# Kernel optimization log

Measured on AMD Instinct MI355X. Metric: run time of the kernel, lower is better.

Reference implementation:

```python
import jax, jax.numpy as jnp
import numpy as np


def setup_inputs() -> dict:
    key = jax.random.key(0)
    k1, k2, k3 = jax.random.split(key, 3)
    B, T, D, H = 64, 512, 1024, 1024
    x = jax.random.normal(k1, (B, T, D), dtype=jnp.float32)
    state = jnp.zeros((B, H), dtype=jnp.float32)
    W = jax.random.normal(k2, (H, H), dtype=jnp.float32) / np.sqrt(H).astype(np.float32)
    U = jax.random.normal(k3, (D, H), dtype=jnp.float32) / np.sqrt(D).astype(np.float32)
    b = jnp.zeros((H,), dtype=jnp.float32)
    return {"x": x, "state": state, "W": W, "U": U, "b": b}


def reference(x, state, W, U, b):
    # x: (B, T, D) -> precompute input projection for all steps: (T, B, H)
    xU = jnp.einsum('btd,dh->tbh', x, U) + b

    def step(h, xu_t):
        h = jnp.tanh(xu_t + h @ W)
        return h, h

    final_state, outs = jax.lax.scan(step, state, xU)  # outs: (T, B, H)
    outs = jnp.transpose(outs, (1, 0, 2))  # (B, T, H)
    return outs, final_state
```

## Files before the change

### kernel.cpp

```cpp
#include <hip/hip_runtime.h>
#include <hip/hip_fp16.h>

typedef float  f4v __attribute__((ext_vector_type(4)));
typedef _Float16 h8v __attribute__((ext_vector_type(8)));
typedef _Float16 h4v __attribute__((ext_vector_type(4)));

#define B_ 64
#define T_ 512
#define H_ 1024

__global__ __launch_bounds__(256) void k_transpose_cvt(const float* __restrict__ src,
                                                       _Float16* __restrict__ dst) {
  __shared__ _Float16 tile[64][72];
  int r0 = blockIdx.y * 64, c0 = blockIdx.x * 64;
  int t = threadIdx.x;
  for (int i = 0; i < 4; ++i) {
    int r = i * 16 + (t >> 4);
    int c = (t & 15) * 4;
    f4v v = *reinterpret_cast<const f4v*>(src + (long)(r0 + r) * 1024 + c0 + c);
    tile[c + 0][r] = (_Float16)v.x;
    tile[c + 1][r] = (_Float16)v.y;
    tile[c + 2][r] = (_Float16)v.z;
    tile[c + 3][r] = (_Float16)v.w;
  }
  __syncthreads();
  for (int i = 0; i < 2; ++i) {
    int rr = i * 32 + (t >> 3);
    int cc = (t & 7) * 8;
    *reinterpret_cast<h8v*>(dst + (long)(c0 + rr) * 1024 + r0 + cc) =
        *reinterpret_cast<const h8v*>(&tile[rr][cc]);
  }
}

#define SWZG(r, kh) ((((r) * 64) + ((kh) * 2)) ^ (((r) & 3) << 4))

__global__ __launch_bounds__(256) void k_gemm_xu(const float* __restrict__ x,
                                                 const _Float16* __restrict__ Ut,
                                                 const float* __restrict__ bias,
                                                 float* __restrict__ out) {
  __shared__ __attribute__((aligned(16))) unsigned char Asm[128 * 32 * 2];
  __shared__ __attribute__((aligned(16))) unsigned char Bsm[128 * 32 * 2];
  int bid = blockIdx.x;
  int nt = bid & 7, mt = bid >> 3;
  int t = threadIdx.x;
  int row = t >> 1, kc = (t & 1) * 16;
  long gA = (long)(mt * 128 + row) * 1024 + kc;
  long gB = (long)(nt * 128 + row) * 1024 + kc;
  int wid = t >> 6, lane = t & 63;
  int wr = (wid >> 1) * 64, wc = (wid & 1) * 64;
  int l15 = lane & 15, khi = (lane >> 4) * 8;

  f4v acc[4][4];
  for (int i = 0; i < 4; ++i)
    for (int j = 0; j < 4; ++j) acc[i][j] = (f4v){0.f, 0.f, 0.f, 0.f};

  f4v ra[4];
  h8v rb[2];
  {
    const float* ap = x + gA;
    ra[0] = *(const f4v*)(ap);     ra[1] = *(const f4v*)(ap + 4);
    ra[2] = *(const f4v*)(ap + 8); ra[3] = *(const f4v*)(ap + 12);
    const _Float16* bp = Ut + gB;
    rb[0] = *(const h8v*)(bp);     rb[1] = *(const h8v*)(bp + 8);
  }
  for (int kt = 0; kt < 32; ++kt) {
    h8v ah0, ah1;
    for (int j = 0; j < 4; ++j) {
      ah0[j]     = (_Float16)ra[0][j];
      ah0[j + 4] = (_Float16)ra[1][j];
      ah1[j]     = (_Float16)ra[2][j];
      ah1[j + 4] = (_Float16)ra[3][j];
    }
    *(h8v*)(Asm + SWZG(row, kc))     = ah0;
    *(h8v*)(Asm + SWZG(row, kc + 8)) = ah1;
    *(h8v*)(Bsm + SWZG(row, kc))     = rb[0];
    *(h8v*)(Bsm + SWZG(row, kc + 8)) = rb[1];
    __syncthreads();
    if (kt < 31) {
      const float* ap = x + gA + (kt + 1) * 32;
      ra[0] = *(const f4v*)(ap);     ra[1] = *(const f4v*)(ap + 4);
      ra[2] = *(const f4v*)(ap + 8); ra[3] = *(const f4v*)(ap + 12);
      const _Float16* bp = Ut + gB + (kt + 1) * 32;
      rb[0] = *(const h8v*)(bp);     rb[1] = *(const h8v*)(bp + 8);
    }
    h8v af[4], bf[4];
    for (int mi = 0; mi < 4; ++mi)
      af[mi] = *(const h8v*)(Asm + SWZG(wr + mi * 16 + l15, khi));
    for (int ni = 0; ni < 4; ++ni)
      bf[ni] = *(const h8v*)(Bsm + SWZG(wc + ni * 16 + l15, khi));
    for (int mi = 0; mi < 4; ++mi)
      for (int ni = 0; ni < 4; ++ni)
        acc[mi][ni] = __builtin_amdgcn_mfma_f32_16x16x32_f16(af[mi], bf[ni], acc[mi][ni], 0, 0, 0);
    __syncthreads();
  }
  int coff = nt * 128 + wc, roff = mt * 128 + wr;
  for (int ni = 0; ni < 4; ++ni) {
    int col = coff + ni * 16 + l15;
    float bb = bias[col];
    for (int mi = 0; mi < 4; ++mi) {
      int rbase = roff + mi * 16 + (lane >> 4) * 4;
      for (int j = 0; j < 4; ++j)
        out[(long)(rbase + j) * 1024 + col] = acc[mi][ni][j] + bb;
    }
  }
}

#define SWZS(r, kh) ((((r) * 2048) + ((kh) * 2)) ^ (((r) & 7) << 4))

__global__ __launch_bounds__(256) void k_scan(const float* __restrict__ state,
                                              float* __restrict__ out,
                                              const _Float16* __restrict__ Wt,
                                              unsigned* __restrict__ ctr) {
  extern __shared__ __attribute__((aligned(16))) unsigned char smem[];
  unsigned char* Wl = smem;
  unsigned char* Hl0 = smem + 65536;
  __shared__ int fastflag;
  int t = threadIdx.x;
  int bid = blockIdx.x;
  int cl = bid & 7;
  int mm = bid >> 3;

  unsigned* stepc = ctr + cl * 32;
  unsigned* testc = ctr + 256 + cl * 32;
  unsigned* gbar  = ctr + 512;

  {
    int r = t >> 3, c8 = t & 7;
    const _Float16* wsrc = Wt + (long)(mm * 32 + r) * 1024;
    for (int j = 0; j < 16; ++j) {
      int kh = (c8 + 8 * j) * 8;
      *(h8v*)(Wl + SWZS(r, kh)) = *(const h8v*)(wsrc + kh);
    }
  }

  if (t == 0) {
    unsigned one = 1u, zero = 0u, got;
    asm volatile("global_atomic_add %0, %1, off\n\ts_waitcnt vmcnt(0)"
                 :: "v"(testc), "v"(one) : "memory");
    __hip_atomic_fetch_add(gbar, 1u, __ATOMIC_RELAXED, __HIP_MEMORY_SCOPE_AGENT);
    while (__hip_atomic_load(gbar, __ATOMIC_RELAXED, __HIP_MEMORY_SCOPE_AGENT) < 256u)
      __builtin_amdgcn_s_sleep(2);
    asm volatile("global_atomic_add %0, %1, %2, off sc0\n\ts_waitcnt vmcnt(0)"
                 : "=&v"(got) : "v"(testc), "v"(zero) : "memory");
    fastflag = (got == 32u);
  }
  __syncthreads();
  const bool fastm = (fastflag != 0);

  int wid = t >> 6, lane = t & 63;
  int srow = t >> 5, slane = t & 31;
  long b = cl * 8 + srow;
  int l15 = lane & 15, khi8 = (lane >> 4) * 8;
  int arow = lane & 7;
  int bro = wid * 16 + l15;
  int hi = lane >> 4;
  int gcol = mm * 32 + wid * 16 + l15;
  bool prod = (wid < 2) && (hi < 2);

  for (int step = 0; step < T_; ++step) {
    unsigned char* Hb = Hl0 + (step & 1) * 16384;

    float xuv[4];
    long addr0 = 0;
    if (prod) {
      addr0 = ((long)(cl * 8 + hi * 4) * T_ + step) * 1024 + gcol;
#pragma unroll
      for (int j = 0; j < 4; ++j) xuv[j] = out[addr0 + (long)j * T_ * 1024];
    }

    if (step == 0) {
      const float* hp0 = state + b * 1024 + slane * 4;
#pragma unroll
      for (int j = 0; j < 8; ++j) {
        f4v v = *(const f4v*)(hp0 + 128 * j);
        h4v hv = {(_Float16)v.x, (_Float16)v.y, (_Float16)v.z, (_Float16)v.w};
        *(h4v*)(Hb + SWZS(srow, (slane + 32 * j) * 4)) = hv;
      }
    } else {
      if (t == 0) {
        unsigned tgt = 32u * (unsigned)step;
        if (fastm) {
          unsigned cur, zero = 0u;
          do {
            asm volatile("global_atomic_add %0, %1, %2, off sc0\n\ts_waitcnt vmcnt(0)"
                         : "=&v"(cur) : "v"(stepc), "v"(zero) : "memory");
          } while (cur < tgt);
        } else {
          while (__hip_atomic_load(stepc, __ATOMIC_RELAXED, __HIP_MEMORY_SCOPE_AGENT) < tgt)
            __builtin_amdgcn_s_sleep(1);
        }
      }
      __syncthreads();

      const float* hrow = out + (b * T_ + (step - 1)) * 1024;
      if (fastm) {
#pragma unroll
        for (int j = 0; j < 8; ++j) {
          int c0 = (slane + 32 * j) * 4;
          if ((c0 >> 5) == mm) continue;
          f4v v = *(const f4v*)(hrow + c0);
          h4v hv = {(_Float16)v.x, (_Float16)v.y, (_Float16)v.z, (_Float16)v.w};
          *(h4v*)(Hb + SWZS(srow, c0)) = hv;
        }
      } else {
        const float* hp = hrow + slane * 4;
        f4v w0, w1, w2, w3, w4, w5, w6, w7;
        asm volatile(
            "global_load_dwordx4 %0, %8, off sc0 sc1\n\t"
            "global_load_dwordx4 %1, %8, off offset:512 sc0 sc1\n\t"
            "global_load_dwordx4 %2, %8, off offset:1024 sc0 sc1\n\t"
            "global_load_dwordx4 %3, %8, off offset:1536 sc0 sc1\n\t"
            "global_load_dwordx4 %4, %8, off offset:2048 sc0 sc1\n\t"
            "global_load_dwordx4 %5, %8, off offset:2560 sc0 sc1\n\t"
            "global_load_dwordx4 %6, %8, off offset:3072 sc0 sc1\n\t"
            "global_load_dwordx4 %7, %8, off offset:3584 sc0 sc1\n\t"
            "s_waitcnt vmcnt(0)"
            : "=&v"(w0), "=&v"(w1), "=&v"(w2), "=&v"(w3),
              "=&v"(w4), "=&v"(w5), "=&v"(w6), "=&v"(w7)
            : "v"(hp)
            : "memory");
        f4v wv[8] = {w0, w1, w2, w3, w4, w5, w6, w7};
#pragma unroll
        for (int j = 0; j < 8; ++j) {
          int c0 = (slane + 32 * j) * 4;
          h4v hv = {(_Float16)wv[j][0], (_Float16)wv[j][1],
                    (_Float16)wv[j][2], (_Float16)wv[j][3]};
          *(h4v*)(Hb + SWZS(srow, c0)) = hv;
        }
      }
    }
    __syncthreads();

    if (wid < 2) {
      f4v ac0 = (f4v){0.f, 0.f, 0.f, 0.f}, ac1 = ac0, ac2 = ac0, ac3 = ac0;
#pragma unroll
      for (int s = 0; s < 32; s += 4) {
        int k0 = s * 32 + khi8, k1 = k0 + 32, k2 = k0 + 64, k3 = k0 + 96;
        h8v af0 = *(const h8v*)(Hb + SWZS(arow, k0));
        h8v bf0 = *(const h8v*)(Wl + SWZS(bro, k0));
        h8v af1 = *(const h8v*)(Hb + SWZS(arow, k1));
        h8v bf1 = *(const h8v*)(Wl + SWZS(bro, k1));
        h8v af2 = *(const h8v*)(Hb + SWZS(arow, k2));
        h8v bf2 = *(const h8v*)(Wl + SWZS(bro, k2));
        h8v af3 = *(const h8v*)(Hb + SWZS(arow, k3));
        h8v bf3 = *(const h8v*)(Wl + SWZS(bro, k3));
        ac0 = __builtin_amdgcn_mfma_f32_16x16x32_f16(af0, bf0, ac0, 0, 0, 0);
        ac1 = __builtin_amdgcn_mfma_f32_16x16x32_f16(af1, bf1, ac1, 0, 0, 0);
        ac2 = __builtin_amdgcn_mfma_f32_16x16x32_f16(af2, bf2, ac2, 0, 0, 0);
        ac3 = __builtin_amdgcn_mfma_f32_16x16x32_f16(af3, bf3, ac3, 0, 0, 0);
      }
      f4v acc = (ac0 + ac1) + (ac2 + ac3);
      if (hi < 2) {
        float v0 = tanhf(acc[0] + xuv[0]);
        float v1 = tanhf(acc[1] + xuv[1]);
        float v2 = tanhf(acc[2] + xuv[2]);
        float v3 = tanhf(acc[3] + xuv[3]);
        float* p0 = out + addr0;
        float* p1 = p0 + (long)T_ * 1024;
        float* p2 = p1 + (long)T_ * 1024;
        float* p3 = p2 + (long)T_ * 1024;
        if (fastm) {
          p0[0] = v0; p1[0] = v1; p2[0] = v2; p3[0] = v3;
        } else {
          asm volatile(
              "global_store_dword %0, %4, off sc0 sc1\n\t"
              "global_store_dword %1, %5, off sc0 sc1\n\t"
              "global_store_dword %2, %6, off sc0 sc1\n\t"
              "global_store_dword %3, %7, off sc0 sc1\n\t"
              "s_waitcnt vmcnt(0)"
              :: "v"(p0), "v"(p1), "v"(p2), "v"(p3),
                 "v"(v0), "v"(v1), "v"(v2), "v"(v3)
              : "memory");
        }
        if (step < T_ - 1) {
          unsigned char* Hn = Hl0 + ((step + 1) & 1) * 16384;
          int cb = gcol & ~3, co = (gcol & 3) * 2;
          int r0r = hi * 4;
          *(_Float16*)(Hn + SWZS(r0r + 0, cb) + co) = (_Float16)v0;
          *(_Float16*)(Hn + SWZS(r0r + 1, cb) + co) = (_Float16)v1;
          *(_Float16*)(Hn + SWZS(r0r + 2, cb) + co) = (_Float16)v2;
          *(_Float16*)(Hn + SWZS(r0r + 3, cb) + co) = (_Float16)v3;
        }
        if (step == T_ - 1) {
          long r = (long)cl * 8 + hi * 4;
          float* q = out + (long)B_ * T_ * 1024 + r * 1024 + gcol;
          q[0] = v0; q[1024] = v1; q[2048] = v2; q[3072] = v3;
        }
      }
    }

    if (prod) {
      asm volatile("s_waitcnt vmcnt(0)" ::: "memory");
    }
    __syncthreads();
    if (t == 0) {
      if (fastm) {
        unsigned one = 1u;
        asm volatile("global_atomic_add %0, %1, off" :: "v"(stepc), "v"(one) : "memory");
      } else {
        __hip_atomic_fetch_add(stepc, 1u, __ATOMIC_RELAXED, __HIP_MEMORY_SCOPE_AGENT);
      }
    }
  }
}

extern "C" void kernel_launch(void* const* d_in, const int* in_sizes, int n_in,
                              void* d_out, int out_size, void* d_ws, size_t ws_size,
                              hipStream_t stream) {
  const float* x     = (const float*)d_in[0];
  const float* state = (const float*)d_in[1];
  const float* W     = (const float*)d_in[2];
  const float* U     = (const float*)d_in[3];
  const float* bias  = (const float*)d_in[4];
  float* out = (float*)d_out;
  unsigned char* ws = (unsigned char*)d_ws;

  _Float16* Ut = (_Float16*)ws;
  _Float16* Wt = (_Float16*)(ws + (1u << 21));
  unsigned* ctr = (unsigned*)(ws + (1u << 22));

  hipMemsetAsync(ctr, 0, 4096, stream);

  k_transpose_cvt<<<dim3(16, 16), 256, 0, stream>>>(U, Ut);
  k_transpose_cvt<<<dim3(16, 16), 256, 0, stream>>>(W, Wt);
  k_gemm_xu<<<2048, 256, 0, stream>>>(x, Ut, bias, out);

  hipFuncSetAttribute((const void*)k_scan, hipFuncAttributeMaxDynamicSharedMemorySize, 98304);
  void* args[] = {(void*)&state, (void*)&out, (void*)&Wt, (void*)&ctr};
  hipLaunchCooperativeKernel((void*)k_scan, dim3(256), dim3(256), args, 98304, stream);
}
```

Before: 1.880 ms.

## Replace per-step counter polling with sharded counters and leader-broadcast flags

In the fast path, the per-cluster step barrier changes. Arrivals are spread across four counters instead of one. Only block mm==0 polls those counters, then writes a per-block flag that the other 31 blocks spin on. This cuts atomic contention from 32 pollers hammering one address, but it adds an extra hop of latency through the leader's flag writes. The final step also skips its arrival increment.

```diff
diff --git a/kernel.cpp b/kernel.cpp
--- a/kernel.cpp
+++ b/kernel.cpp
@@ -120,9 +120,12 @@
   int cl = bid & 7;
   int mm = bid >> 3;
 
-  unsigned* stepc = ctr + cl * 32;
-  unsigned* testc = ctr + 256 + cl * 32;
-  unsigned* gbar  = ctr + 512;
+  unsigned* stepc  = ctr + cl * 32;
+  unsigned* testc  = ctr + 256 + cl * 32;
+  unsigned* gbar   = ctr + 512;
+  unsigned* fc     = ctr + 1024 + cl * 128;
+  unsigned* flbase = ctr + 2048 + cl * 1024;
+  unsigned* myflag = flbase + mm * 32;
 
   {
     int r = t >> 3, c8 = t & 7;
@@ -180,11 +183,30 @@
       if (t == 0) {
         unsigned tgt = 32u * (unsigned)step;
         if (fastm) {
-          unsigned cur, zero = 0u;
-          do {
-            asm volatile("global_atomic_add %0, %1, %2, off sc0\n\ts_waitcnt vmcnt(0)"
-                         : "=&v"(cur) : "v"(stepc), "v"(zero) : "memory");
-          } while (cur < tgt);
+          unsigned zero = 0u;
+          if (mm == 0) {
+            unsigned c0, c1, c2, c3;
+            for (;;) {
+              asm volatile(
+                  "global_atomic_add %0, %5, %4, off sc0\n\t"
+                  "global_atomic_add %1, %6, %4, off sc0\n\t"
+                  "global_atomic_add %2, %7, %4, off sc0\n\t"
+                  "global_atomic_add %3, %8, %4, off sc0\n\t"
+                  "s_waitcnt vmcnt(0)"
+                  : "=&v"(c0), "=&v"(c1), "=&v"(c2), "=&v"(c3)
+                  : "v"(zero), "v"(fc), "v"(fc + 32), "v"(fc + 64), "v"(fc + 96)
+                  : "memory");
+              if (c0 + c1 + c2 + c3 >= tgt) break;
+            }
+            volatile unsigned* fl = (volatile unsigned*)flbase;
+            for (int m = 1; m < 32; ++m) fl[m * 32] = (unsigned)step;
+          } else {
+            unsigned cur;
+            do {
+              asm volatile("global_atomic_add %0, %1, %2, off sc0\n\ts_waitcnt vmcnt(0)"
+                           : "=&v"(cur) : "v"(myflag), "v"(zero) : "memory");
+            } while (cur < (unsigned)step);
+          }
         } else {
           while (__hip_atomic_load(stepc, __ATOMIC_RELAXED, __HIP_MEMORY_SCOPE_AGENT) < tgt)
             __builtin_amdgcn_s_sleep(1);
@@ -293,10 +315,11 @@
       asm volatile("s_waitcnt vmcnt(0)" ::: "memory");
     }
     __syncthreads();
-    if (t == 0) {
+    if (t == 0 && step < T_ - 1) {
       if (fastm) {
         unsigned one = 1u;
-        asm volatile("global_atomic_add %0, %1, off" :: "v"(stepc), "v"(one) : "memory");
+        unsigned* myc = fc + (mm & 3) * 32;
+        asm volatile("global_atomic_add %0, %1, off" :: "v"(myc), "v"(one) : "memory");
       } else {
         __hip_atomic_fetch_add(stepc, 1u, __ATOMIC_RELAXED, __HIP_MEMORY_SCOPE_AGENT);
       }
@@ -319,7 +342,7 @@
   _Float16* Wt = (_Float16*)(ws + (1u << 21));
   unsigned* ctr = (unsigned*)(ws + (1u << 22));
 
-  hipMemsetAsync(ctr, 0, 4096, stream);
+  hipMemsetAsync(ctr, 0, 40960, stream);
 
   k_transpose_cvt<<<dim3(16, 16), 256, 0, stream>>>(U, Ut);
   k_transpose_cvt<<<dim3(16, 16), 256, 0, stream>>>(W, Wt);
```

Measured after the change: 6.502 ms. 3.46x slower.
